# Kernel optimization log

Measured on AMD Instinct MI355X. Metric: run time of the kernel, lower is better.

## Reference

```python
import jax, jax.numpy as jnp
import numpy as np

EPS = 1e-12  # matches torch F.normalize default eps
SCALE = 64.0  # fixed softmax temperature from the source

def _l2_normalize(x, axis):
    n = jnp.linalg.norm(x, ord=2, axis=axis, keepdims=True)
    return x / jnp.maximum(n, EPS)

def setup_inputs() -> dict:
    key = jax.random.key(0)
    k1, k2, k3 = jax.random.split(key, 3)
    B, L, S, D = 8, 2048, 2048, 128
    return {
        "query": jax.random.normal(k1, (B, L, D), dtype=jnp.float32),
        "key": jax.random.normal(k2, (B, S, D), dtype=jnp.float32),
        "value": jax.random.normal(k3, (B, S, D), dtype=jnp.float32),
    }

def reference(query, key, value):
    # rank-3 query path with norm=True, return_value=True, return_score=False
    q = _l2_normalize(query, axis=2)   # [B, L, D]
    k = _l2_normalize(key, axis=2)     # [B, S, D]
    score = jnp.einsum('nlk,nsk->nls', q, k)            # [B, L, S]
    score = jax.nn.softmax(score * SCALE, axis=2)
    # original does broadcast-multiply-then-sum; equivalent contraction:
    out = jnp.einsum('nls,nsd->nld', score, value)      # [B, L, D]
    return out
```

## Files before the change

kernel.cpp:

```cpp
#include <hip/hip_runtime.h>
#include <stdint.h>

#define Bb 8
#define Ll 2048
#define Ss 2048
#define Dd 128
#define NSB 4
#define SCHUNK 512
#define NROWS 16384
#define SCALE_LOG2E 92.33248261689366f

typedef __attribute__((ext_vector_type(8))) short bf16x8;
typedef __attribute__((ext_vector_type(16))) float f32x16;

__device__ __forceinline__ unsigned f2bf_pack(float a, float b) {
  unsigned ua = __float_as_uint(a); ua += 0x7fffu + ((ua >> 16) & 1u);
  unsigned ub = __float_as_uint(b); ub += 0x7fffu + ((ub >> 16) & 1u);
  return (ua >> 16) | (ub & 0xffff0000u);
}

__device__ __forceinline__ unsigned pkbf(float a, float b) {
#if __has_builtin(__builtin_amdgcn_cvt_pk_bf16_f32)
  auto r = __builtin_amdgcn_cvt_pk_bf16_f32(a, b);
  return __builtin_bit_cast(unsigned, r);
#else
  return f2bf_pack(a, b);
#endif
}

__device__ __forceinline__ void gl_lds16(const void* g, void* l) {
  __builtin_amdgcn_global_load_lds(
      (const __attribute__((address_space(1))) unsigned*)g,
      (__attribute__((address_space(3))) unsigned*)l, 16, 0, 0);
}


extern "C" __global__ __launch_bounds__(256)
void prep_kern(const float* __restrict__ Q, const float* __restrict__ K,
               const float* __restrict__ V,
               unsigned short* __restrict__ Qn, unsigned short* __restrict__ Kf,
               unsigned short* __restrict__ Vf) {
  __shared__ float Tf[32 * 130];
  __shared__ float Ps[32 * 8];
  __shared__ float Nr[32];
  __shared__ unsigned short Tb[32 * 128];
  const int t = threadIdx.x;
  const int bid = blockIdx.x;
  if (bid < 4096) {
    const int lane = t & 63;
    const int r = bid * 4 + (t >> 6);
    float2 f = *(const float2*)(Q + (size_t)r * Dd + lane * 2);
    float ss = f.x * f.x + f.y * f.y;
#pragma unroll
    for (int m = 1; m < 64; m <<= 1) ss += __shfl_xor(ss, m, 64);
    float inv = 1.0f / fmaxf(sqrtf(ss), 1e-12f);
    *(unsigned*)(Qn + (size_t)r * Dd + lane * 2) = pkbf(f.x * inv, f.y * inv);
  } else if (bid < 4608) {
    const int kb = bid - 4096;
    const int b = kb & 7, sw = kb >> 3;
    const int sl = t >> 3, d0 = (t & 7) * 16;
    const float* src = K + ((size_t)(b * Ss + sw * 32 + sl)) * Dd + d0;
    float ss = 0.f;
#pragma unroll
    for (int i = 0; i < 4; ++i) {
      float4 v = *(const float4*)(src + i * 4);
      Tf[sl * 130 + d0 + i * 4 + 0] = v.x;
      Tf[sl * 130 + d0 + i * 4 + 1] = v.y;
      Tf[sl * 130 + d0 + i * 4 + 2] = v.z;
      Tf[sl * 130 + d0 + i * 4 + 3] = v.w;
      ss += v.x * v.x + v.y * v.y + v.z * v.z + v.w * v.w;
    }
    Ps[sl * 8 + (t & 7)] = ss;
    __syncthreads();
    if (t < 32) {
      float s = 0.f;
#pragma unroll
      for (int j = 0; j < 8; ++j) s += Ps[t * 8 + j];
      Nr[t] = 1.0f / fmaxf(sqrtf(s), 1e-12f);
    }
    __syncthreads();
    unsigned short* Ko = Kf + ((size_t)(b * 64 + sw)) * 4096;
#pragma unroll
    for (int p = 0; p < 2; ++p) {
      const int run = p * 256 + t;
      const int lane = run & 63, s = lane & 31, h = lane >> 5;
      const int d = (run >> 6) * 16 + h * 8;
      const float n = Nr[s];
      const float* row = &Tf[s * 130 + d];
      uint4 w;
      w.x = pkbf(row[0] * n, row[1] * n);
      w.y = pkbf(row[2] * n, row[3] * n);
      w.z = pkbf(row[4] * n, row[5] * n);
      w.w = pkbf(row[6] * n, row[7] * n);
      *(uint4*)(Ko + run * 8) = w;
    }
  } else {
    const int vb = bid - 4608;
    const int b = vb & 7, sw = vb >> 3;
    const int sl = t >> 3, d0 = (t & 7) * 16;
    const float* src = V + ((size_t)(b * Ss + sw * 32 + sl)) * Dd + d0;
#pragma unroll
    for (int i = 0; i < 4; ++i) {
      float4 v = *(const float4*)(src + i * 4);
      *(unsigned*)&Tb[sl * 128 + d0 + i * 4]     = pkbf(v.x, v.y);
      *(unsigned*)&Tb[sl * 128 + d0 + i * 4 + 2] = pkbf(v.z, v.w);
    }
    __syncthreads();
    unsigned short* Vo = Vf + ((size_t)(b * 64 + sw)) * 4096;
#pragma unroll
    for (int p = 0; p < 2; ++p) {
      const int run = p * 256 + t;
      const int vslot = run >> 6, lane = run & 63;
      const int dloc = lane & 31, h = lane >> 5;
      const int dblk = vslot >> 1, t2 = vslot & 1;
      const int d = dblk * 32 + dloc;
      unsigned short w[8];
#pragma unroll
      for (int j = 0; j < 8; ++j) {
        const int sloc = t2 * 16 + 4 * h + (j & 3) + 8 * (j >> 2);
        w[j] = Tb[sloc * 128 + d];
      }
      *(uint4*)(Vo + run * 8) = *(uint4*)w;
    }
  }
}

extern "C" __global__ __launch_bounds__(256, 2)
void attn_kern(const unsigned short* __restrict__ Qn,
               const unsigned short* __restrict__ Kf,
               const unsigned short* __restrict__ Vf,
               unsigned short* __restrict__ Op,
               float* __restrict__ Lp) {
  __shared__ unsigned short Kl[4][8 * 512];
  __shared__ unsigned short Vl[4][8 * 512];
  const int tid = threadIdx.x, wv = tid >> 6, lane = tid & 63;
  const int lm = lane & 31, h = lane >> 5;
  const int gid = blockIdx.x;
  const int qt = gid >> 5, b = (gid >> 2) & 7, sb = gid & 3;
  const int sblk0 = sb * (SCHUNK / 32);
  const int qrow = qt * 128 + wv * 32 + lm;

  const unsigned short* Qrow = Qn + ((size_t)(b * Ll + qrow)) * Dd;
  bf16x8 qf[8];
#pragma unroll
  for (int kt = 0; kt < 8; ++kt)
    qf[kt] = *(const bf16x8*)(Qrow + kt * 16 + h * 8);

  const unsigned short* Kc = Kf + ((size_t)(b * 64 + sblk0)) * 4096;
  const unsigned short* Vc = Vf + ((size_t)(b * 64 + sblk0)) * 4096;

  f32x16 o[4];
#pragma unroll
  for (int i = 0; i < 4; ++i)
#pragma unroll
    for (int r = 0; r < 16; ++r) o[i][r] = 0.f;

  auto stage = [&](int t, int r) {
    const unsigned short* kb = Kc + (size_t)t * 4096;
    const unsigned short* vb = Vc + (size_t)t * 4096;
#pragma unroll
    for (int i = 0; i < 2; ++i) {
      const int sl = wv * 2 + i;
      gl_lds16(kb + sl * 512 + lane * 8, &Kl[r][sl * 512]);
      gl_lds16(vb + sl * 512 + lane * 8, &Vl[r][sl * 512]);
    }
  };
  stage(0, 0);
  stage(1, 1);

  float lrun = 0.f;

#pragma unroll 1
  for (int it = 0; it < 16; ++it) {
    if (it < 15)
      asm volatile("s_waitcnt vmcnt(4)\n\ts_barrier" ::: "memory");
    else
      asm volatile("s_waitcnt vmcnt(0)\n\ts_barrier" ::: "memory");
    const int r = it & 3;
    if (it + 2 < 16) stage(it + 2, (it + 2) & 3);

    f32x16 acc;
#pragma unroll
    for (int rr = 0; rr < 16; ++rr) acc[rr] = 0.f;
#pragma unroll
    for (int kt = 0; kt < 8; ++kt) {
      bf16x8 kf = *(const bf16x8*)&Kl[r][kt * 512 + lane * 8];
      acc = __builtin_amdgcn_mfma_f32_32x32x16_bf16(kf, qf[kt], acc, 0, 0, 0);
    }
#pragma unroll
    for (int t2 = 0; t2 < 2; ++t2) {
      float p[8];
#pragma unroll
      for (int j = 0; j < 8; ++j)
        p[j] = __builtin_amdgcn_exp2f(
            __builtin_fmaf(acc[t2 * 8 + j], SCALE_LOG2E, -SCALE_LOG2E));
      lrun += ((p[0] + p[1]) + (p[2] + p[3])) + ((p[4] + p[5]) + (p[6] + p[7]));
      uint4 fr;
      fr.x = pkbf(p[0], p[1]);
      fr.y = pkbf(p[2], p[3]);
      fr.z = pkbf(p[4], p[5]);
      fr.w = pkbf(p[6], p[7]);
      bf16x8 pf = __builtin_bit_cast(bf16x8, fr);
#pragma unroll
      for (int dblk = 0; dblk < 4; ++dblk) {
        bf16x8 vf = *(const bf16x8*)&Vl[r][(dblk * 2 + t2) * 512 + lane * 8];
        o[dblk] = __builtin_amdgcn_mfma_f32_32x32x16_bf16(vf, pf, o[dblk], 0, 0, 0);
      }
    }
  }

  const float lt = lrun + __shfl_xor(lrun, 32, 64);
  unsigned short* Ob = Op + ((size_t)sb * NROWS + b * Ll + qrow) * Dd;
#pragma unroll
  for (int dblk = 0; dblk < 4; ++dblk)
#pragma unroll
    for (int g = 0; g < 4; ++g) {
      uint2 w;
      w.x = pkbf(o[dblk][g * 4 + 0], o[dblk][g * 4 + 1]);
      w.y = pkbf(o[dblk][g * 4 + 2], o[dblk][g * 4 + 3]);
      *(uint2*)(Ob + dblk * 32 + g * 8 + h * 4) = w;
    }
  if (h == 0) Lp[sb * NROWS + b * Ll + qrow] = lt;
}

extern "C" __global__ __launch_bounds__(256)
void comb_kern(const unsigned short* __restrict__ Op,
               const float* __restrict__ Lp, float* __restrict__ Out) {
  const int idx = blockIdx.x * 256 + threadIdx.x;
  const int row = idx >> 5;
  const int dof = (idx & 31) * 4;
  float den = 0.f;
#pragma unroll
  for (int s = 0; s < NSB; ++s) den += Lp[s * NROWS + row];
  float a0 = 0.f, a1 = 0.f, a2 = 0.f, a3 = 0.f;
#pragma unroll
  for (int s = 0; s < NSB; ++s) {
    uint2 v = *(const uint2*)(Op + ((size_t)s * NROWS + row) * Dd + dof);
    a0 += __uint_as_float(v.x << 16);
    a1 += __uint_as_float(v.x & 0xffff0000u);
    a2 += __uint_as_float(v.y << 16);
    a3 += __uint_as_float(v.y & 0xffff0000u);
  }
  const float inv = 1.f / den;
  float4 r; r.x = a0 * inv; r.y = a1 * inv; r.z = a2 * inv; r.w = a3 * inv;
  *(float4*)(Out + (size_t)row * Dd + dof) = r;
}

extern "C" void kernel_launch(void* const* d_in, const int* in_sizes, int n_in,
                              void* d_out, int out_size, void* d_ws, size_t ws_size,
                              hipStream_t stream) {
  const float* Q = (const float*)d_in[0];
  const float* K = (const float*)d_in[1];
  const float* V = (const float*)d_in[2];
  float* Out = (float*)d_out;
  unsigned short* Qn = (unsigned short*)d_ws;
  unsigned short* Kf = Qn + (size_t)NROWS * Dd;
  unsigned short* Vf = Kf + (size_t)NROWS * Dd;
  unsigned short* Op = Vf + (size_t)Bb * Dd * Ss;
  float* Lp = (float*)(Op + (size_t)NSB * NROWS * Dd);
  hipLaunchKernelGGL(prep_kern, dim3(4096 + 512 + 512), dim3(256), 0, stream,
                     Q, K, V, Qn, Kf, Vf);
  hipLaunchKernelGGL(attn_kern, dim3(512), dim3(256), 0, stream, Qn, Kf, Vf, Op, Lp);
  hipLaunchKernelGGL(comb_kern, dim3(2048), dim3(256), 0, stream, Op, Lp, Out);
}
```

Measured before the change: 106.6 us.

## Double per-wave query rows so K/V tiles feed twice the MFMAs, halve S chunk

Each wave now handles 64 query rows (two 32-row MFMA tiles) instead of 32. Every K/V fragment loaded from LDS is therefore reused for two MFMAs, which halves LDS and global K/V traffic per unit of work. The S split goes from 4 chunks of 512 to 8 chunks of 256 to keep the grid size the same. The change also adds s_setprio around the MFMA phases. In exchange it needs more registers (16 Q fragments, 8 output accumulators), which may limit occupancy under launch_bounds(256,2), and the combine kernel has to read twice as many bf16 partials.

After: 114.8 us. 1.08x slower.

```diff
diff --git a/kernel.cpp b/kernel.cpp
--- a/kernel.cpp
+++ b/kernel.cpp
@@ -5,8 +5,8 @@
 #define Ll 2048
 #define Ss 2048
 #define Dd 128
-#define NSB 4
-#define SCHUNK 512
+#define NSB 8
+#define SCHUNK 256
 #define NROWS 16384
 #define SCALE_LOG2E 92.33248261689366f
 
@@ -136,22 +136,25 @@
   const int tid = threadIdx.x, wv = tid >> 6, lane = tid & 63;
   const int lm = lane & 31, h = lane >> 5;
   const int gid = blockIdx.x;
-  const int qt = gid >> 5, b = (gid >> 2) & 7, sb = gid & 3;
-  const int sblk0 = sb * (SCHUNK / 32);
-  const int qrow = qt * 128 + wv * 32 + lm;
-
-  const unsigned short* Qrow = Qn + ((size_t)(b * Ll + qrow)) * Dd;
-  bf16x8 qf[8];
-#pragma unroll
-  for (int kt = 0; kt < 8; ++kt)
-    qf[kt] = *(const bf16x8*)(Qrow + kt * 16 + h * 8);
-
-  const unsigned short* Kc = Kf + ((size_t)(b * 64 + sblk0)) * 4096;
-  const unsigned short* Vc = Vf + ((size_t)(b * 64 + sblk0)) * 4096;
-
-  f32x16 o[4];
-#pragma unroll
-  for (int i = 0; i < 4; ++i)
+  const int sb = gid >> 6, qt = (gid >> 3) & 7, b = gid & 7;
+  const int qrow0 = qt * 256 + wv * 64;
+
+  bf16x8 qf[16];
+#pragma unroll
+  for (int mh = 0; mh < 2; ++mh) {
+    const unsigned short* Qrow =
+        Qn + ((size_t)(b * Ll + qrow0 + mh * 32 + lm)) * Dd;
+#pragma unroll
+    for (int kt = 0; kt < 8; ++kt)
+      qf[mh * 8 + kt] = *(const bf16x8*)(Qrow + kt * 16 + h * 8);
+  }
+
+  const unsigned short* Kc = Kf + ((size_t)(b * 64 + sb * 8)) * 4096;
+  const unsigned short* Vc = Vf + ((size_t)(b * 64 + sb * 8)) * 4096;
+
+  f32x16 o[8];
+#pragma unroll
+  for (int i = 0; i < 8; ++i)
 #pragma unroll
     for (int r = 0; r < 16; ++r) o[i][r] = 0.f;
 
@@ -168,59 +171,84 @@
   stage(0, 0);
   stage(1, 1);
 
-  float lrun = 0.f;
+  float lr0 = 0.f, lr1 = 0.f;
 
 #pragma unroll 1
-  for (int it = 0; it < 16; ++it) {
-    if (it < 15)
+  for (int it = 0; it < 8; ++it) {
+    if (it < 7)
       asm volatile("s_waitcnt vmcnt(4)\n\ts_barrier" ::: "memory");
     else
       asm volatile("s_waitcnt vmcnt(0)\n\ts_barrier" ::: "memory");
     const int r = it & 3;
-    if (it + 2 < 16) stage(it + 2, (it + 2) & 3);
-
-    f32x16 acc;
-#pragma unroll
-    for (int rr = 0; rr < 16; ++rr) acc[rr] = 0.f;
+    if (it + 2 < 8) stage(it + 2, (it + 2) & 3);
+
+    f32x16 a0, a1;
+#pragma unroll
+    for (int rr = 0; rr < 16; ++rr) { a0[rr] = 0.f; a1[rr] = 0.f; }
+    __builtin_amdgcn_s_setprio(1);
 #pragma unroll
     for (int kt = 0; kt < 8; ++kt) {
       bf16x8 kf = *(const bf16x8*)&Kl[r][kt * 512 + lane * 8];
-      acc = __builtin_amdgcn_mfma_f32_32x32x16_bf16(kf, qf[kt], acc, 0, 0, 0);
-    }
+      a0 = __builtin_amdgcn_mfma_f32_32x32x16_bf16(kf, qf[kt], a0, 0, 0, 0);
+      a1 = __builtin_amdgcn_mfma_f32_32x32x16_bf16(kf, qf[8 + kt], a1, 0, 0, 0);
+    }
+    __builtin_amdgcn_s_setprio(0);
+
+    uint4 pf0[2], pf1[2];
 #pragma unroll
     for (int t2 = 0; t2 < 2; ++t2) {
-      float p[8];
-#pragma unroll
-      for (int j = 0; j < 8; ++j)
+      float p[8], q[8];
+#pragma unroll
+      for (int j = 0; j < 8; ++j) {
         p[j] = __builtin_amdgcn_exp2f(
-            __builtin_fmaf(acc[t2 * 8 + j], SCALE_LOG2E, -SCALE_LOG2E));
-      lrun += ((p[0] + p[1]) + (p[2] + p[3])) + ((p[4] + p[5]) + (p[6] + p[7]));
-      uint4 fr;
-      fr.x = pkbf(p[0], p[1]);
-      fr.y = pkbf(p[2], p[3]);
-      fr.z = pkbf(p[4], p[5]);
-      fr.w = pkbf(p[6], p[7]);
-      bf16x8 pf = __builtin_bit_cast(bf16x8, fr);
+            __builtin_fmaf(a0[t2 * 8 + j], SCALE_LOG2E, -SCALE_LOG2E));
+        q[j] = __builtin_amdgcn_exp2f(
+            __builtin_fmaf(a1[t2 * 8 + j], SCALE_LOG2E, -SCALE_LOG2E));
+      }
+      lr0 += ((p[0] + p[1]) + (p[2] + p[3])) + ((p[4] + p[5]) + (p[6] + p[7]));
+      lr1 += ((q[0] + q[1]) + (q[2] + q[3])) + ((q[4] + q[5]) + (q[6] + q[7]));
+      pf0[t2].x = pkbf(p[0], p[1]);
+      pf0[t2].y = pkbf(p[2], p[3]);
+      pf0[t2].z = pkbf(p[4], p[5]);
+      pf0[t2].w = pkbf(p[6], p[7]);
+      pf1[t2].x = pkbf(q[0], q[1]);
+      pf1[t2].y = pkbf(q[2], q[3]);
+      pf1[t2].z = pkbf(q[4], q[5]);
+      pf1[t2].w = pkbf(q[6], q[7]);
+    }
+
+    __builtin_amdgcn_s_setprio(1);
+#pragma unroll
+    for (int t2 = 0; t2 < 2; ++t2) {
 #pragma unroll
       for (int dblk = 0; dblk < 4; ++dblk) {
         bf16x8 vf = *(const bf16x8*)&Vl[r][(dblk * 2 + t2) * 512 + lane * 8];
-        o[dblk] = __builtin_amdgcn_mfma_f32_32x32x16_bf16(vf, pf, o[dblk], 0, 0, 0);
-      }
-    }
-  }
-
-  const float lt = lrun + __shfl_xor(lrun, 32, 64);
-  unsigned short* Ob = Op + ((size_t)sb * NROWS + b * Ll + qrow) * Dd;
-#pragma unroll
-  for (int dblk = 0; dblk < 4; ++dblk)
-#pragma unroll
-    for (int g = 0; g < 4; ++g) {
-      uint2 w;
-      w.x = pkbf(o[dblk][g * 4 + 0], o[dblk][g * 4 + 1]);
-      w.y = pkbf(o[dblk][g * 4 + 2], o[dblk][g * 4 + 3]);
-      *(uint2*)(Ob + dblk * 32 + g * 8 + h * 4) = w;
-    }
-  if (h == 0) Lp[sb * NROWS + b * Ll + qrow] = lt;
+        o[dblk] = __builtin_amdgcn_mfma_f32_32x32x16_bf16(
+            vf, __builtin_bit_cast(bf16x8, pf0[t2]), o[dblk], 0, 0, 0);
+        o[4 + dblk] = __builtin_amdgcn_mfma_f32_32x32x16_bf16(
+            vf, __builtin_bit_cast(bf16x8, pf1[t2]), o[4 + dblk], 0, 0, 0);
+      }
+    }
+    __builtin_amdgcn_s_setprio(0);
+  }
+
+#pragma unroll
+  for (int mh = 0; mh < 2; ++mh) {
+    const float lrm = mh ? lr1 : lr0;
+    const float lt = lrm + __shfl_xor(lrm, 32, 64);
+    const int qr = qrow0 + mh * 32 + lm;
+    unsigned short* Ob = Op + ((size_t)sb * NROWS + b * Ll + qr) * Dd;
+#pragma unroll
+    for (int dblk = 0; dblk < 4; ++dblk)
+#pragma unroll
+      for (int g = 0; g < 4; ++g) {
+        uint2 w;
+        w.x = pkbf(o[mh * 4 + dblk][g * 4 + 0], o[mh * 4 + dblk][g * 4 + 1]);
+        w.y = pkbf(o[mh * 4 + dblk][g * 4 + 2], o[mh * 4 + dblk][g * 4 + 3]);
+        *(uint2*)(Ob + dblk * 32 + g * 8 + h * 4) = w;
+      }
+    if (h == 0) Lp[(size_t)sb * NROWS + b * Ll + qr] = lt;
+  }
 }
 
 extern "C" __global__ __launch_bounds__(256)
@@ -231,7 +259,7 @@
   const int dof = (idx & 31) * 4;
   float den = 0.f;
 #pragma unroll
-  for (int s = 0; s < NSB; ++s) den += Lp[s * NROWS + row];
+  for (int s = 0; s < NSB; ++s) den += Lp[(size_t)s * NROWS + row];
   float a0 = 0.f, a1 = 0.f, a2 = 0.f, a3 = 0.f;
 #pragma unroll
   for (int s = 0; s < NSB; ++s) {
```

## Fuse query normalization into attention kernel and widen combine vector loads

Applied to the files above, without the earlier changes.

Query L2 normalization and bf16 conversion move out of the prep kernel and into the attention kernel. Each lane loads its fp32 query slice, computes a partial sum of squares, and reduces across the two half-waves. This drops the Qn workspace write and read, and the prep grid shrinks to only the K/V blocks. Each attention block now reads fp32 queries, twice the bytes of the bf16 copy. The combine kernel also processes 8 elements per thread with 16-byte loads and half as many blocks.

New measurement: 107.5 us. Within noise of the previous version (+0.8%).

```diff
diff --git a/kernel.cpp b/kernel.cpp
--- a/kernel.cpp
+++ b/kernel.cpp
@@ -36,27 +36,16 @@
 
 
 extern "C" __global__ __launch_bounds__(256)
-void prep_kern(const float* __restrict__ Q, const float* __restrict__ K,
-               const float* __restrict__ V,
-               unsigned short* __restrict__ Qn, unsigned short* __restrict__ Kf,
-               unsigned short* __restrict__ Vf) {
+void prep_kern(const float* __restrict__ K, const float* __restrict__ V,
+               unsigned short* __restrict__ Kf, unsigned short* __restrict__ Vf) {
   __shared__ float Tf[32 * 130];
   __shared__ float Ps[32 * 8];
   __shared__ float Nr[32];
   __shared__ unsigned short Tb[32 * 128];
   const int t = threadIdx.x;
   const int bid = blockIdx.x;
-  if (bid < 4096) {
-    const int lane = t & 63;
-    const int r = bid * 4 + (t >> 6);
-    float2 f = *(const float2*)(Q + (size_t)r * Dd + lane * 2);
-    float ss = f.x * f.x + f.y * f.y;
-#pragma unroll
-    for (int m = 1; m < 64; m <<= 1) ss += __shfl_xor(ss, m, 64);
-    float inv = 1.0f / fmaxf(sqrtf(ss), 1e-12f);
-    *(unsigned*)(Qn + (size_t)r * Dd + lane * 2) = pkbf(f.x * inv, f.y * inv);
-  } else if (bid < 4608) {
-    const int kb = bid - 4096;
+  if (bid < 512) {
+    const int kb = bid;
     const int b = kb & 7, sw = kb >> 3;
     const int sl = t >> 3, d0 = (t & 7) * 16;
     const float* src = K + ((size_t)(b * Ss + sw * 32 + sl)) * Dd + d0;
@@ -95,7 +84,7 @@
       *(uint4*)(Ko + run * 8) = w;
     }
   } else {
-    const int vb = bid - 4608;
+    const int vb = bid - 512;
     const int b = vb & 7, sw = vb >> 3;
     const int sl = t >> 3, d0 = (t & 7) * 16;
     const float* src = V + ((size_t)(b * Ss + sw * 32 + sl)) * Dd + d0;
@@ -126,7 +115,7 @@
 }
 
 extern "C" __global__ __launch_bounds__(256, 2)
-void attn_kern(const unsigned short* __restrict__ Qn,
+void attn_kern(const float* __restrict__ Q,
                const unsigned short* __restrict__ Kf,
                const unsigned short* __restrict__ Vf,
                unsigned short* __restrict__ Op,
@@ -140,11 +129,31 @@
   const int sblk0 = sb * (SCHUNK / 32);
   const int qrow = qt * 128 + wv * 32 + lm;
 
-  const unsigned short* Qrow = Qn + ((size_t)(b * Ll + qrow)) * Dd;
+  const float* Qr = Q + ((size_t)(b * Ll + qrow)) * Dd;
+  float qv[8][8];
+  float ss = 0.f;
+#pragma unroll
+  for (int kt = 0; kt < 8; ++kt) {
+    const float* cp = Qr + kt * 16 + h * 8;
+    float4 u0 = *(const float4*)cp;
+    float4 u1 = *(const float4*)(cp + 4);
+    qv[kt][0] = u0.x; qv[kt][1] = u0.y; qv[kt][2] = u0.z; qv[kt][3] = u0.w;
+    qv[kt][4] = u1.x; qv[kt][5] = u1.y; qv[kt][6] = u1.z; qv[kt][7] = u1.w;
+    ss += u0.x * u0.x + u0.y * u0.y + u0.z * u0.z + u0.w * u0.w +
+          u1.x * u1.x + u1.y * u1.y + u1.z * u1.z + u1.w * u1.w;
+  }
+  ss += __shfl_xor(ss, 32, 64);
+  const float qinv = 1.0f / fmaxf(sqrtf(ss), 1e-12f);
   bf16x8 qf[8];
 #pragma unroll
-  for (int kt = 0; kt < 8; ++kt)
-    qf[kt] = *(const bf16x8*)(Qrow + kt * 16 + h * 8);
+  for (int kt = 0; kt < 8; ++kt) {
+    uint4 w;
+    w.x = pkbf(qv[kt][0] * qinv, qv[kt][1] * qinv);
+    w.y = pkbf(qv[kt][2] * qinv, qv[kt][3] * qinv);
+    w.z = pkbf(qv[kt][4] * qinv, qv[kt][5] * qinv);
+    w.w = pkbf(qv[kt][6] * qinv, qv[kt][7] * qinv);
+    qf[kt] = __builtin_bit_cast(bf16x8, w);
+  }
 
   const unsigned short* Kc = Kf + ((size_t)(b * 64 + sblk0)) * 4096;
   const unsigned short* Vc = Vf + ((size_t)(b * 64 + sblk0)) * 4096;
@@ -227,23 +236,30 @@
 void comb_kern(const unsigned short* __restrict__ Op,
                const float* __restrict__ Lp, float* __restrict__ Out) {
   const int idx = blockIdx.x * 256 + threadIdx.x;
-  const int row = idx >> 5;
-  const int dof = (idx & 31) * 4;
+  const int row = idx >> 4;
+  const int dof = (idx & 15) * 8;
   float den = 0.f;
 #pragma unroll
   for (int s = 0; s < NSB; ++s) den += Lp[s * NROWS + row];
-  float a0 = 0.f, a1 = 0.f, a2 = 0.f, a3 = 0.f;
+  float a[8] = {0.f, 0.f, 0.f, 0.f, 0.f, 0.f, 0.f, 0.f};
 #pragma unroll
   for (int s = 0; s < NSB; ++s) {
-    uint2 v = *(const uint2*)(Op + ((size_t)s * NROWS + row) * Dd + dof);
-    a0 += __uint_as_float(v.x << 16);
-    a1 += __uint_as_float(v.x & 0xffff0000u);
-    a2 += __uint_as_float(v.y << 16);
-    a3 += __uint_as_float(v.y & 0xffff0000u);
+    uint4 v = *(const uint4*)(Op + ((size_t)s * NROWS + row) * Dd + dof);
+    a[0] += __uint_as_float(v.x << 16);
+    a[1] += __uint_as_float(v.x & 0xffff0000u);
+    a[2] += __uint_as_float(v.y << 16);
+    a[3] += __uint_as_float(v.y & 0xffff0000u);
+    a[4] += __uint_as_float(v.z << 16);
+    a[5] += __uint_as_float(v.z & 0xffff0000u);
+    a[6] += __uint_as_float(v.w << 16);
+    a[7] += __uint_as_float(v.w & 0xffff0000u);
   }
   const float inv = 1.f / den;
-  float4 r; r.x = a0 * inv; r.y = a1 * inv; r.z = a2 * inv; r.w = a3 * inv;
-  *(float4*)(Out + (size_t)row * Dd + dof) = r;
+  float4 r0; r0.x = a[0] * inv; r0.y = a[1] * inv; r0.z = a[2] * inv; r0.w = a[3] * inv;
+  float4 r1; r1.x = a[4] * inv; r1.y = a[5] * inv; r1.z = a[6] * inv; r1.w = a[7] * inv;
+  float* op = Out + (size_t)row * Dd + dof;
+  *(float4*)op = r0;
+  *(float4*)(op + 4) = r1;
 }
 
 extern "C" void kernel_launch(void* const* d_in, const int* in_sizes, int n_in,
@@ -253,13 +269,11 @@
   const float* K = (const float*)d_in[1];
   const float* V = (const float*)d_in[2];
   float* Out = (float*)d_out;
-  unsigned short* Qn = (unsigned short*)d_ws;
-  unsigned short* Kf = Qn + (size_t)NROWS * Dd;
+  unsigned short* Kf = (unsigned short*)d_ws;
   unsigned short* Vf = Kf + (size_t)NROWS * Dd;
   unsigned short* Op = Vf + (size_t)Bb * Dd * Ss;
   float* Lp = (float*)(Op + (size_t)NSB * NROWS * Dd);
-  hipLaunchKernelGGL(prep_kern, dim3(4096 + 512 + 512), dim3(256), 0, stream,
-                     Q, K, V, Qn, Kf, Vf);
-  hipLaunchKernelGGL(attn_kern, dim3(512), dim3(256), 0, stream, Qn, Kf, Vf, Op, Lp);
-  hipLaunchKernelGGL(comb_kern, dim3(2048), dim3(256), 0, stream, Op, Lp, Out);
-}
+  hipLaunchKernelGGL(prep_kern, dim3(1024), dim3(256), 0, stream, K, V, Kf, Vf);
+  hipLaunchKernelGGL(attn_kern, dim3(512), dim3(256), 0, stream, Q, Kf, Vf, Op, Lp);
+  hipLaunchKernelGGL(comb_kern, dim3(1024), dim3(256), 0, stream, Op, Lp, Out);
+}
```
